# Performance work log

Measured on AMD Instinct MI355X. Metric: run time of the kernel, lower is better.

The kernel has to match this reference:

```python
import jax, jax.numpy as jnp
import numpy as np

N_VISITS, N_PROC, N_MED = 64, 32, 16
V_DIAG, V_PROC, V_MED = 2000, 1500, 4000
EMB, EMB_FF = 256, 128


def _normalize(adj):
    # row-normalize(adj + I), matching GCN.normalize
    adj = adj + np.eye(adj.shape[0], dtype=np.float32)
    rs = adj.sum(1)
    rinv = np.where(rs > 0, 1.0 / rs, 0.0).astype(np.float32)
    return (adj * rinv[:, None]).astype(np.float32)


def setup_inputs() -> dict:
    key = jax.random.key(0)
    ks = jax.random.split(key, 24)
    rng = np.random.default_rng(0)
    ehr = (rng.random((V_MED, V_MED)) < 0.01).astype(np.float32)
    ddi = (rng.random((V_MED, V_MED)) < 0.01).astype(np.float32)
    s = 0.02
    return {
        'proc_codes': jax.random.randint(ks[0], (N_VISITS, N_PROC), 0, V_DIAG + V_PROC + 2),
        'med_codes': jax.random.randint(ks[1], (N_VISITS, N_MED), 0, V_MED),
        'emb_table': jax.random.normal(ks[2], (V_DIAG + V_PROC + 2, EMB_FF)) * s,
        'conv_w': jax.random.normal(ks[3], (3,)) * 0.3,
        'conv_b': jnp.zeros((1,)),
        'wq': jax.random.normal(ks[4], (EMB_FF, EMB)) * s,
        'wk': jax.random.normal(ks[5], (EMB_FF, EMB)) * s,
        'wv': jax.random.normal(ks[6], (EMB_FF, EMB)) * s,
        'wr': jax.random.normal(ks[7], (EMB, EMB)) * s,
        'alpha': jax.random.normal(ks[8], (EMB,)),
        'beta': jax.random.normal(ks[9], (EMB,)),
        'ehr_adj_norm': jnp.asarray(_normalize(ehr)),
        'ddi_adj_norm': jnp.asarray(_normalize(ddi)),
        'ddi_adj_raw': jnp.asarray(ddi),
        'ehr_w1': jax.random.normal(ks[10], (V_MED, EMB)) * s,
        'ehr_b1': jnp.zeros((EMB,)),
        'ehr_w2': jax.random.normal(ks[11], (EMB, EMB)) * s,
        'ehr_b2': jnp.zeros((EMB,)),
        'ddi_w1': jax.random.normal(ks[12], (V_MED, EMB)) * s,
        'ddi_b1': jnp.zeros((EMB,)),
        'ddi_w2': jax.random.normal(ks[13], (EMB, EMB)) * s,
        'ddi_b2': jnp.zeros((EMB,)),
        'inter': jax.random.normal(ks[14], (1,)) * 0.1,
        'out_w1': jax.random.normal(ks[15], (3 * EMB, 2 * EMB)) * s,
        'out_b1': jnp.zeros((2 * EMB,)),
        'out_w2': jax.random.normal(ks[16], (2 * EMB, V_MED)) * s,
        'out_b2': jnp.zeros((V_MED,)),
    }


def _fastformer(x, wq, wk, wv, wr, alpha, beta):
    # x: (1, n, EMB_FF); additive linear attention (all-ones mask => no-op)
    q = x @ wq  # (1, n, EMB)
    k = x @ wk
    v = x @ wv
    scale = EMB ** -0.5
    aw = jax.nn.softmax(q * alpha * scale, axis=-1)
    gq = jnp.sum(q * aw, axis=1)              # global query (1, EMB)
    p = gq[:, None, :] * k                    # (1, n, EMB)
    bw = jax.nn.softmax(p * beta * scale, axis=-1)
    gk = jnp.sum(p * bw, axis=1)              # global key (1, EMB)
    return (gk[:, None, :] * v) @ wr + q


def _gcn(adj, w1, b1, w2, b2):
    # input x = I, so first layer support is just w1
    h = jax.nn.relu(adj @ w1 + b1)
    return adj @ (h @ w2) + b2


def reference(proc_codes, med_codes, emb_table, conv_w, conv_b, wq, wk, wv, wr, alpha, beta,
              ehr_adj_norm, ddi_adj_norm, ddi_adj_raw,
              ehr_w1, ehr_b1, ehr_w2, ehr_b2, ddi_w1, ddi_b1, ddi_w2, ddi_b2,
              inter, out_w1, out_b1, out_w2, out_b2):
    n = proc_codes.shape[0]
    # per-admission mean embedding  (n, EMB_FF)
    i2 = emb_table[proc_codes].mean(axis=1)
    # Conv1d(1,1,k=3,same) over the feature dim, then ReLU
    xp = jnp.pad(i2, ((0, 0), (1, 1)))
    i2 = jax.nn.relu(conv_w[0] * xp[:, :-2] + conv_w[1] * xp[:, 1:-1] + conv_w[2] * xp[:, 2:] + conv_b)
    feat = _fastformer(i2[None], wq, wk, wv, wr, alpha, beta)[0]  # (n, EMB)
    query = feat[-1:]
    drug_memory = _gcn(ehr_adj_norm, ehr_w1, ehr_b1, ehr_w2, ehr_b2) \
        - _gcn(ddi_adj_norm, ddi_w1, ddi_b1, ddi_w2, ddi_b2) * inter[0]
    key_w1 = jax.nn.softmax(query @ drug_memory.T, axis=-1)   # (1, V_MED)
    fact1 = key_w1 @ drug_memory                              # (1, EMB)
    # history (len(input) > 1): multi-hot med history values
    history_keys = feat[:-1]
    hv = jnp.zeros((n - 1, V_MED), dtype=feat.dtype)
    hv = hv.at[jnp.arange(n - 1)[:, None], med_codes[:-1]].set(1.0)
    visit_w = jax.nn.softmax(query @ history_keys.T, axis=-1)
    fact2 = (visit_w @ hv) @ drug_memory
    h = jnp.concatenate([query, fact1, fact2], axis=-1)       # (1, 3*EMB)
    result = jax.nn.relu(h @ out_w1 + out_b1) @ out_w2 + out_b2
    sp = jax.nn.sigmoid(result)[0]
    batch_neg = 0.0005 * jnp.einsum('i,ij,j->', sp, ddi_adj_raw, sp)
    return result, batch_neg
```

## Files before the change

kernel.cpp:

```cpp
#include <hip/hip_runtime.h>
#include <hip/hip_bf16.h>

#define NV 64
#define NP 32
#define NM 16
#define VMED 4000
#define EMB 256
#define EMBFF 128
#define CAP 128


__device__ __forceinline__ float block_sum_256(float v, float* red) {
    int t = threadIdx.x;
    red[t] = v; __syncthreads();
    for (int s = 128; s > 0; s >>= 1) { if (t < s) red[t] += red[t + s]; __syncthreads(); }
    float r = red[0]; __syncthreads();
    return r;
}
__device__ __forceinline__ float block_max_256(float v, float* red) {
    int t = threadIdx.x;
    red[t] = v; __syncthreads();
    for (int s = 128; s > 0; s >>= 1) { if (t < s) red[t] = fmaxf(red[t], red[t + s]); __syncthreads(); }
    float r = red[0]; __syncthreads();
    return r;
}

__global__ void k_ff1(const int* __restrict__ proc, const float* __restrict__ emb,
                      const float* __restrict__ cw, const float* __restrict__ cb,
                      const float* __restrict__ wq, const float* __restrict__ wk,
                      const float* __restrict__ wv, const float* __restrict__ alpha,
                      float* __restrict__ q, float* __restrict__ k, float* __restrict__ v,
                      float* __restrict__ qaw) {
    __shared__ float sm[EMBFF + 2];
    __shared__ float x[EMBFF];
    __shared__ float red[256];
    int vi = blockIdx.x, t = threadIdx.x;
    if (t < EMBFF) {
        float s = 0.f;
        for (int c = 0; c < NP; c++) s += emb[proc[vi * NP + c] * EMBFF + t];
        sm[t + 1] = s * (1.0f / NP);
    }
    if (t == 0) { sm[0] = 0.f; sm[EMBFF + 1] = 0.f; }
    __syncthreads();
    if (t < EMBFF) {
        float o = cw[0] * sm[t] + cw[1] * sm[t + 1] + cw[2] * sm[t + 2] + cb[0];
        x[t] = o > 0.f ? o : 0.f;
    }
    __syncthreads();
    float aq = 0, ak = 0, av = 0;
    for (int e = 0; e < EMBFF; e++) {
        float xe = x[e];
        aq += xe * wq[e * EMB + t];
        ak += xe * wk[e * EMB + t];
        av += xe * wv[e * EMB + t];
    }
    q[vi * EMB + t] = aq; k[vi * EMB + t] = ak; v[vi * EMB + t] = av;
    const float scale = 0.0625f;
    float z = aq * alpha[t] * scale;
    float m = block_max_256(z, red);
    float e_ = __expf(z - m);
    float sum = block_sum_256(e_, red);
    qaw[vi * EMB + t] = aq * (e_ / sum);
}

__global__ void k_pbw(const float* __restrict__ qaw, const float* __restrict__ k,
                      const float* __restrict__ beta, float* __restrict__ pbw) {
    __shared__ float red[256];
    int vi = blockIdx.x, f = threadIdx.x;
    float g = 0;
    for (int r = 0; r < NV; r++) g += qaw[r * EMB + f];
    float p = g * k[vi * EMB + f];
    const float scale = 0.0625f;
    float z = p * beta[f] * scale;
    float m = block_max_256(z, red);
    float e_ = __expf(z - m);
    float sum = block_sum_256(e_, red);
    pbw[vi * EMB + f] = p * (e_ / sum);
}

__global__ void k_feat(const float* __restrict__ pbw, const float* __restrict__ v,
                       const float* __restrict__ q, const float* __restrict__ wr,
                       float* __restrict__ feat) {
    __shared__ float s[EMB];
    int vi = blockIdx.x, f = threadIdx.x;
    float g = 0;
    for (int r = 0; r < NV; r++) g += pbw[r * EMB + f];
    s[f] = g * v[vi * EMB + f];
    __syncthreads();
    float acc = 0;
    for (int e = 0; e < EMB; e++) acc += s[e] * wr[e * EMB + f];
    feat[vi * EMB + f] = acc + q[vi * EMB + f];
}

__global__ void k_visitw_wmed(const float* __restrict__ feat, const int* __restrict__ med,
                              float* __restrict__ w_med) {
    __shared__ float qs[EMB];
    __shared__ float vw[64];
    __shared__ float red[256];
    __shared__ float wm[VMED];
    int t = threadIdx.x;
    for (int e = t; e < EMB; e += 256) qs[e] = feat[63 * EMB + e];
    for (int i = t; i < VMED; i += 256) wm[i] = 0.f;
    __syncthreads();
    float sc = -1e30f;
    if (t < 63) {
        float a = 0;
        for (int e = 0; e < EMB; e++) a += qs[e] * feat[t * EMB + e];
        sc = a;
    }
    float m = block_max_256(sc, red);
    float e_ = (t < 63) ? __expf(sc - m) : 0.f;
    float sum = block_sum_256(e_, red);
    if (t < 63) vw[t] = e_ / sum;
    __syncthreads();
    for (int i = t; i < 63 * NM; i += 256) {
        int vv = i / NM, mm = i % NM;
        int code = med[vv * NM + mm];
        bool dup = false;
        for (int m2 = 0; m2 < mm; m2++)
            if (med[vv * NM + m2] == code) dup = true;
        if (!dup) atomicAdd(&wm[code], vw[vv]);
    }
    __syncthreads();
    for (int i = t; i < VMED; i += 256) w_med[i] = wm[i];
}

__global__ void k_scan(const float* __restrict__ eadj, const float* __restrict__ draw,
                       int* __restrict__ ccntE, int* __restrict__ cidxE, float* __restrict__ cvalE,
                       int* __restrict__ ccntD, int* __restrict__ cidxD, float* __restrict__ cvalD) {
    __shared__ int idx[CAP];
    __shared__ float val[CAP];
    __shared__ int cnt;
    int b = blockIdx.x, t = threadIdx.x;
    bool isD = b >= VMED;
    int i = isD ? b - VMED : b;
    const float* adj = isD ? draw : eadj;
    int*   ccnt = isD ? ccntD : ccntE;
    int*   cidx = isD ? cidxD : cidxE;
    float* cval = isD ? cvalD : cvalE;
    if (t == 0) cnt = 0;
    const float4* row4 = (const float4*)(adj + (size_t)i * VMED);
    float4 a0 = row4[t];
    float4 a1 = row4[t + 256];
    float4 a2 = row4[t + 512];
    float4 a3 = (t < VMED / 4 - 768) ? row4[t + 768] : make_float4(0.f, 0.f, 0.f, 0.f);
    asm volatile("" :: "v"(a0.x), "v"(a0.y), "v"(a0.z), "v"(a0.w),
                       "v"(a1.x), "v"(a1.y), "v"(a1.z), "v"(a1.w),
                       "v"(a2.x), "v"(a2.y), "v"(a2.z), "v"(a2.w),
                       "v"(a3.x), "v"(a3.y), "v"(a3.z), "v"(a3.w));
    __syncthreads();
    #define PROC(A, C0) \
        if (A.x != 0.f) { int p = atomicAdd(&cnt, 1); if (p < CAP) { idx[p] = (C0);     val[p] = A.x; } } \
        if (A.y != 0.f) { int p = atomicAdd(&cnt, 1); if (p < CAP) { idx[p] = (C0) + 1; val[p] = A.y; } } \
        if (A.z != 0.f) { int p = atomicAdd(&cnt, 1); if (p < CAP) { idx[p] = (C0) + 2; val[p] = A.z; } } \
        if (A.w != 0.f) { int p = atomicAdd(&cnt, 1); if (p < CAP) { idx[p] = (C0) + 3; val[p] = A.w; } }
    PROC(a0, t * 4)
    PROC(a1, (t + 256) * 4)
    PROC(a2, (t + 512) * 4)
    PROC(a3, (t + 768) * 4)
    #undef PROC
    __syncthreads();
    int n;
    float rinv = 0.f;
    if (isD) {
        int n_raw = cnt < CAP - 1 ? cnt : CAP - 1;
        n = n_raw + 1;
        rinv = 1.0f / (float)n;
        if (t == n_raw) { idx[t] = i; }
    } else {
        n = cnt < CAP ? cnt : CAP;
    }
    __syncthreads();
    int n8 = (n + 7) & ~7;
    if (t == 0) ccnt[i] = n;
    if (t < n)       { cidx[i * CAP + t] = idx[t]; cval[i * CAP + t] = isD ? rinv : val[t]; }
    else if (t < n8) { cidx[i * CAP + t] = 0;      cval[i * CAP + t] = 0.f; }
}

__global__ void k_gat(const int* __restrict__ ccntE, const int* __restrict__ cidxE,
                      const float* __restrict__ cvalE,
                      const int* __restrict__ ccntD, const int* __restrict__ cidxD,
                      const float* __restrict__ cvalD,
                      const float* __restrict__ ew1, const float* __restrict__ eb1,
                      const float* __restrict__ dw1, const float* __restrict__ db1,
                      float* __restrict__ hE, float* __restrict__ hD) {
    int b = blockIdx.x, t = threadIdx.x;
    bool isD = (b & 4) != 0;
    int rank = (b >> 3) * 4 + (b & 3);
    const int*   ccnt = isD ? ccntD : ccntE;
    const int*   cidx = isD ? cidxD : cidxE;
    const float* cval = isD ? cvalD : cvalE;
    const float* w1   = isD ? dw1 : ew1;
    const float* b1   = isD ? db1 : eb1;
    float* h = isD ? hD : hE;
    int r0 = rank * 4;
    for (int r = 0; r < 4; r++) {
        int base = (r0 + r) * CAP;
        int n8 = (ccnt[r0 + r] + 7) & ~7;
        float acc = b1[t];
        for (int e = 0; e < n8; e += 8) {
            int i0 = cidx[base + e];     float v0 = cval[base + e];
            int i1 = cidx[base + e + 1]; float v1 = cval[base + e + 1];
            int i2 = cidx[base + e + 2]; float v2 = cval[base + e + 2];
            int i3 = cidx[base + e + 3]; float v3 = cval[base + e + 3];
            int i4 = cidx[base + e + 4]; float v4 = cval[base + e + 4];
            int i5 = cidx[base + e + 5]; float v5 = cval[base + e + 5];
            int i6 = cidx[base + e + 6]; float v6 = cval[base + e + 6];
            int i7 = cidx[base + e + 7]; float v7 = cval[base + e + 7];
            acc += v0 * w1[(size_t)i0 * EMB + t] + v1 * w1[(size_t)i1 * EMB + t]
                 + v2 * w1[(size_t)i2 * EMB + t] + v3 * w1[(size_t)i3 * EMB + t]
                 + v4 * w1[(size_t)i4 * EMB + t] + v5 * w1[(size_t)i5 * EMB + t]
                 + v6 * w1[(size_t)i6 * EMB + t] + v7 * w1[(size_t)i7 * EMB + t];
        }
        h[(size_t)(r0 + r) * EMB + t] = acc > 0.f ? acc : 0.f;
    }
}

__global__ void k_gemm2(const float* __restrict__ ew2, const float* __restrict__ dw2,
                        float* __restrict__ hE, float* __restrict__ hD) {
    __shared__ __align__(16) float x[EMB][12];
    int b = blockIdx.x, t = threadIdx.x;
    bool isD = (b & 4) != 0;
    int rank = (b >> 3) * 4 + (b & 3);
    const float* w2 = isD ? dw2 : ew2;
    float* h = isD ? hD : hE;
    int r0 = rank * 8;
    #pragma unroll
    for (int rr = 0; rr < 8; rr++)
        x[t][rr] = h[(size_t)(r0 + rr) * EMB + t];
    __syncthreads();
    float a0 = 0, a1 = 0, a2 = 0, a3 = 0, a4 = 0, a5 = 0, a6 = 0, a7 = 0;
    #pragma unroll 4
    for (int e = 0; e < EMB; e++) {
        float we = w2[e * EMB + t];
        float4 xa = *(const float4*)&x[e][0];
        float4 xb = *(const float4*)&x[e][4];
        a0 += xa.x * we; a1 += xa.y * we; a2 += xa.z * we; a3 += xa.w * we;
        a4 += xb.x * we; a5 += xb.y * we; a6 += xb.z * we; a7 += xb.w * we;
    }
    h[(size_t)(r0 + 0) * EMB + t] = a0;
    h[(size_t)(r0 + 1) * EMB + t] = a1;
    h[(size_t)(r0 + 2) * EMB + t] = a2;
    h[(size_t)(r0 + 3) * EMB + t] = a3;
    h[(size_t)(r0 + 4) * EMB + t] = a4;
    h[(size_t)(r0 + 5) * EMB + t] = a5;
    h[(size_t)(r0 + 6) * EMB + t] = a6;
    h[(size_t)(r0 + 7) * EMB + t] = a7;
}

__global__ void k_accE(const int* __restrict__ ccntE, const int* __restrict__ cidxE,
                       const float* __restrict__ cvalE, const float* __restrict__ xe,
                       const float* __restrict__ b2e, float* __restrict__ dm) {
    __shared__ int idxE[CAP];
    __shared__ float valE[CAP];
    int i = blockIdx.x, t = threadIdx.x;
    int nE = ccntE[i];
    int nE8 = (nE + 7) & ~7;
    if (t < nE) { idxE[t] = cidxE[i * CAP + t]; valE[t] = cvalE[i * CAP + t]; }
    else if (t < nE8) { idxE[t] = 0; valE[t] = 0.f; }
    __syncthreads();
    float aE = b2e[t];
    for (int e = 0; e < nE8; e += 8) {
        float g0 = xe[(size_t)idxE[e]     * EMB + t];
        float g1 = xe[(size_t)idxE[e + 1] * EMB + t];
        float g2 = xe[(size_t)idxE[e + 2] * EMB + t];
        float g3 = xe[(size_t)idxE[e + 3] * EMB + t];
        float g4 = xe[(size_t)idxE[e + 4] * EMB + t];
        float g5 = xe[(size_t)idxE[e + 5] * EMB + t];
        float g6 = xe[(size_t)idxE[e + 6] * EMB + t];
        float g7 = xe[(size_t)idxE[e + 7] * EMB + t];
        aE += valE[e] * g0 + valE[e + 1] * g1 + valE[e + 2] * g2 + valE[e + 3] * g3
            + valE[e + 4] * g4 + valE[e + 5] * g5 + valE[e + 6] * g6 + valE[e + 7] * g7;
    }
    dm[(size_t)i * EMB + t] = aE;
}

__global__ void k_accD(const int* __restrict__ ccntD, const int* __restrict__ cidxD,
                       const float* __restrict__ cvalD, const float* __restrict__ xd,
                       const float* __restrict__ b2d, const float* __restrict__ inter,
                       const float* __restrict__ feat, float* __restrict__ dm,
                       float* __restrict__ sdm) {
    __shared__ int idxD[CAP];
    __shared__ float valD[CAP];
    __shared__ float red[256];
    int i = blockIdx.x, t = threadIdx.x;
    int nD = ccntD[i];
    int nD8 = (nD + 7) & ~7;
    if (t < nD) { idxD[t] = cidxD[i * CAP + t]; valD[t] = cvalD[i * CAP + t]; }
    else if (t < nD8) { idxD[t] = 0; valD[t] = 0.f; }
    __syncthreads();
    float aD = b2d[t];
    for (int e = 0; e < nD8; e += 8) {
        float g0 = xd[(size_t)idxD[e]     * EMB + t];
        float g1 = xd[(size_t)idxD[e + 1] * EMB + t];
        float g2 = xd[(size_t)idxD[e + 2] * EMB + t];
        float g3 = xd[(size_t)idxD[e + 3] * EMB + t];
        float g4 = xd[(size_t)idxD[e + 4] * EMB + t];
        float g5 = xd[(size_t)idxD[e + 5] * EMB + t];
        float g6 = xd[(size_t)idxD[e + 6] * EMB + t];
        float g7 = xd[(size_t)idxD[e + 7] * EMB + t];
        aD += valD[e] * g0 + valD[e + 1] * g1 + valD[e + 2] * g2 + valD[e + 3] * g3
            + valD[e + 4] * g4 + valD[e + 5] * g5 + valD[e + 6] * g6 + valD[e + 7] * g7;
    }
    float dmv = dm[(size_t)i * EMB + t] - inter[0] * aD;
    dm[(size_t)i * EMB + t] = dmv;
    float s = block_sum_256(dmv * feat[63 * EMB + t], red);
    if (t == 0) sdm[i] = s;
}

__global__ void k_softmax4000(const float* __restrict__ s, float* __restrict__ out) {
    __shared__ float red[256];
    int t = threadIdx.x;
    float m = -1e30f;
    for (int i = t; i < VMED; i += 256) m = fmaxf(m, s[i]);
    m = block_max_256(m, red);
    float sum = 0;
    for (int i = t; i < VMED; i += 256) { float e = __expf(s[i] - m); out[i] = e; sum += e; }
    sum = block_sum_256(sum, red);
    float inv = 1.f / sum;
    for (int i = t; i < VMED; i += 256) out[i] *= inv;
}

__global__ void k_facts_part(const float* __restrict__ dm, const float* __restrict__ kw,
                             const float* __restrict__ wm, float* __restrict__ part1,
                             float* __restrict__ part2) {
    int f = threadIdx.x, b = blockIdx.x;
    int r0 = b * 100;
    float a1 = 0, a2 = 0;
    for (int r = r0; r < r0 + 100; r++) {
        float d = dm[(size_t)r * EMB + f];
        a1 += kw[r] * d;
        a2 += wm[r] * d;
    }
    part1[b * EMB + f] = a1;
    part2[b * EMB + f] = a2;
}

__global__ void k_hidden_part(const float* __restrict__ feat, const float* __restrict__ part1,
                              const float* __restrict__ part2, const float* __restrict__ w1,
                              float* __restrict__ hpart) {
    __shared__ float xs[16];
    int b = blockIdx.x, t = threadIdx.x;
    int e0 = b * 16;
    if (t < 16) {
        int e = e0 + t;
        float xv;
        if (e < 256) xv = feat[63 * EMB + e];
        else if (e < 512) { float s = 0; for (int p = 0; p < 40; p++) s += part1[p * EMB + (e - 256)]; xv = s; }
        else              { float s = 0; for (int p = 0; p < 40; p++) s += part2[p * EMB + (e - 512)]; xv = s; }
        xs[t] = xv;
    }
    __syncthreads();
    float a1 = 0, a2 = 0;
    #pragma unroll
    for (int i = 0; i < 16; i++) {
        int e = e0 + i;
        a1 += xs[i] * w1[e * 512 + t];
        a2 += xs[i] * w1[e * 512 + t + 256];
    }
    hpart[b * 512 + t] = a1;
    hpart[b * 512 + t + 256] = a2;
}

__global__ void k_result(const float* __restrict__ hpart, const float* __restrict__ b1,
                         const float* __restrict__ w2, const float* __restrict__ b2,
                         float* __restrict__ out, float* __restrict__ sp) {
    __shared__ float hx[512];
    __shared__ float red[8][32];
    int t = threadIdx.x;
    for (int jj = t; jj < 512; jj += 256) {
        float s = b1[jj];
        for (int p = 0; p < 48; p++) s += hpart[p * 512 + jj];
        hx[jj] = s > 0.f ? s : 0.f;
    }
    __syncthreads();
    int lane = t & 31, seg = t >> 5;
    int j = blockIdx.x * 32 + lane;
    float acc = 0;
    int e0 = seg * 64;
    #pragma unroll 8
    for (int e = e0; e < e0 + 64; e++) acc += hx[e] * w2[(size_t)e * VMED + j];
    red[seg][lane] = acc;
    __syncthreads();
    if (seg == 0) {
        float s = b2[j];
        for (int p = 0; p < 8; p++) s += red[p][lane];
        out[j] = s;
        sp[j] = 1.f / (1.f + __expf(-s));
    }
}

__global__ void k_bneg(const int* __restrict__ ccntD, const int* __restrict__ cidxD,
                       const float* __restrict__ sp, float* __restrict__ bpart) {
    int wv = threadIdx.x >> 6, lane = threadIdx.x & 63;
    int i = blockIdx.x * 4 + wv;
    int n = ccntD[i] - 1;
    float s = 0.f;
    for (int e = lane; e < n; e += 64) s += sp[cidxD[i * CAP + e]];
    for (int off = 32; off > 0; off >>= 1) s += __shfl_down(s, off, 64);
    if (lane == 0) bpart[i] = sp[i] * s;
}

__global__ void FastRx_wo_Diag_19473381720179_kernel(const float* __restrict__ bpart,
                                                     float* __restrict__ out) {
    __shared__ float red[256];
    int t = threadIdx.x;
    float s = 0;
    for (int i = t; i < VMED; i += 256) s += bpart[i];
    s = block_sum_256(s, red);
    if (t == 0) out[VMED] = 0.0005f * s;
}

extern "C" __attribute__((visibility("default")))
void kernel_launch(void* const* d_in, const int* in_sizes, int n_in,
                   void* d_out, int out_size, void* d_ws, size_t ws_size,
                   hipStream_t stream) {
    const int*   proc_codes = (const int*)d_in[0];
    const int*   med_codes  = (const int*)d_in[1];
    const float* emb_table  = (const float*)d_in[2];
    const float* conv_w     = (const float*)d_in[3];
    const float* conv_b     = (const float*)d_in[4];
    const float* wq         = (const float*)d_in[5];
    const float* wk         = (const float*)d_in[6];
    const float* wv         = (const float*)d_in[7];
    const float* wr         = (const float*)d_in[8];
    const float* alpha      = (const float*)d_in[9];
    const float* beta       = (const float*)d_in[10];
    const float* ehr_adj    = (const float*)d_in[11];
    const float* ddi_adj    = (const float*)d_in[12];
    const float* ddi_raw    = (const float*)d_in[13];
    const float* ehr_w1     = (const float*)d_in[14];
    const float* ehr_b1     = (const float*)d_in[15];
    const float* ehr_w2     = (const float*)d_in[16];
    const float* ehr_b2     = (const float*)d_in[17];
    const float* ddi_w1     = (const float*)d_in[18];
    const float* ddi_b1     = (const float*)d_in[19];
    const float* ddi_w2     = (const float*)d_in[20];
    const float* ddi_b2     = (const float*)d_in[21];
    const float* inter      = (const float*)d_in[22];
    const float* out_w1     = (const float*)d_in[23];
    const float* out_b1     = (const float*)d_in[24];
    const float* out_w2     = (const float*)d_in[25];
    const float* out_b2     = (const float*)d_in[26];
    float* out = (float*)d_out;

    float* w = (float*)d_ws;
    float* q      = w;
    float* k      = w + 16384;
    float* v      = w + 32768;
    float* tmpA   = w + 49152;
    float* tmpB   = w + 65536;
    float* feat   = w + 81920;
    float* wmed   = w + 98304;
    float* sdm    = w + 102400;
    float* sp     = w + 106496;
    float* bufA   = w + 110592;
    float* bufC   = bufA + 1024000;
    float* bufB   = bufC + 1024000;
    int*   ccntE  = (int*)(bufB + 1024000);
    int*   cidxE  = ccntE + 4096;
    float* cvalE  = (float*)(cidxE + 512000);
    int*   ccntD  = (int*)(cvalE + 512000);
    int*   cidxD  = ccntD + 4096;
    float* cvalD  = (float*)(cidxD + 512000);
    float* part1  = bufA;
    float* part2  = bufA + 10240;
    float* hpart  = bufA + 20480;
    float* bpart  = bufA + 45056;

    k_ff1<<<NV, EMB, 0, stream>>>(proc_codes, emb_table, conv_w, conv_b,
                                  wq, wk, wv, alpha, q, k, v, tmpA);
    k_pbw<<<NV, EMB, 0, stream>>>(tmpA, k, beta, tmpB);
    k_feat<<<NV, EMB, 0, stream>>>(tmpB, v, q, wr, feat);
    k_visitw_wmed<<<1, 256, 0, stream>>>(feat, med_codes, wmed);

    k_scan<<<2 * VMED, 256, 0, stream>>>(ehr_adj, ddi_raw,
                                         ccntE, cidxE, cvalE, ccntD, cidxD, cvalD);
    k_gat<<<2000, 256, 0, stream>>>(ccntE, cidxE, cvalE, ccntD, cidxD, cvalD,
                                    ehr_w1, ehr_b1, ddi_w1, ddi_b1,
                                    bufA, bufC);
    k_gemm2<<<1000, 256, 0, stream>>>(ehr_w2, ddi_w2, bufA, bufC);
    k_accE<<<VMED, 256, 0, stream>>>(ccntE, cidxE, cvalE, bufA, ehr_b2, bufB);
    k_accD<<<VMED, 256, 0, stream>>>(ccntD, cidxD, cvalD, bufC, ddi_b2, inter,
                                     feat, bufB, sdm);

    k_softmax4000<<<1, 256, 0, stream>>>(sdm, sdm);
    k_facts_part<<<40, 256, 0, stream>>>(bufB, sdm, wmed, part1, part2);
    k_hidden_part<<<48, 256, 0, stream>>>(feat, part1, part2, out_w1, hpart);
    k_result<<<125, 256, 0, stream>>>(hpart, out_b1, out_w2, out_b2, out, sp);
    k_bneg<<<VMED / 4, 256, 0, stream>>>(ccntD, cidxD, sp, bpart);
    FastRx_wo_Diag_19473381720179_kernel<<<1, 256, 0, stream>>>(bpart, out);
}
```

Before: 396.4 us.

## Merge front and tail kernel chains into cooperative kernels with grid sync

The four fastformer/visit-weight kernels become one cooperative kernel that uses grid.sync between stages. The six tail kernels (softmax, facts, hidden, result, bneg, final reduce) become one cooperative kernel of 125 blocks. The separate E and D accumulation kernels are fused into one, which also drops a dm write and reread. The goal is to cut launch overhead and inter-kernel gaps for many tiny kernels, at the price of grid-wide barrier cost, fewer blocks on some stages, and larger shared memory in the front kernel.

```diff
diff --git a/kernel.cpp b/kernel.cpp
--- a/kernel.cpp
+++ b/kernel.cpp
@@ -1,5 +1,8 @@
 #include <hip/hip_runtime.h>
 #include <hip/hip_bf16.h>
+#include <hip/hip_cooperative_groups.h>
+
+namespace cg = cooperative_groups;
 
 #define NV 64
 #define NP 32
@@ -25,16 +28,25 @@
     return r;
 }
 
-__global__ void k_ff1(const int* __restrict__ proc, const float* __restrict__ emb,
-                      const float* __restrict__ cw, const float* __restrict__ cb,
-                      const float* __restrict__ wq, const float* __restrict__ wk,
-                      const float* __restrict__ wv, const float* __restrict__ alpha,
-                      float* __restrict__ q, float* __restrict__ k, float* __restrict__ v,
-                      float* __restrict__ qaw) {
+__global__ void k_front(const int* __restrict__ proc, const float* __restrict__ emb,
+                        const float* __restrict__ cw, const float* __restrict__ cb,
+                        const float* __restrict__ wq, const float* __restrict__ wk,
+                        const float* __restrict__ wv, const float* __restrict__ alpha,
+                        const float* __restrict__ beta, const float* __restrict__ wr,
+                        const int* __restrict__ med,
+                        float* __restrict__ q, float* __restrict__ k, float* __restrict__ v,
+                        float* __restrict__ qaw, float* __restrict__ pbw,
+                        float* __restrict__ feat, float* __restrict__ w_med) {
     __shared__ float sm[EMBFF + 2];
     __shared__ float x[EMBFF];
     __shared__ float red[256];
+    __shared__ float sfeat[EMB];
+    __shared__ float qs[EMB];
+    __shared__ float vw[64];
+    __shared__ float wm[VMED];
+    cg::grid_group grid = cg::this_grid();
     int vi = blockIdx.x, t = threadIdx.x;
+
     if (t < EMBFF) {
         float s = 0.f;
         for (int c = 0; c < NP; c++) s += emb[proc[vi * NP + c] * EMBFF + t];
@@ -47,82 +59,74 @@
         x[t] = o > 0.f ? o : 0.f;
     }
     __syncthreads();
-    float aq = 0, ak = 0, av = 0;
-    for (int e = 0; e < EMBFF; e++) {
-        float xe = x[e];
-        aq += xe * wq[e * EMB + t];
-        ak += xe * wk[e * EMB + t];
-        av += xe * wv[e * EMB + t];
-    }
-    q[vi * EMB + t] = aq; k[vi * EMB + t] = ak; v[vi * EMB + t] = av;
-    const float scale = 0.0625f;
-    float z = aq * alpha[t] * scale;
-    float m = block_max_256(z, red);
-    float e_ = __expf(z - m);
-    float sum = block_sum_256(e_, red);
-    qaw[vi * EMB + t] = aq * (e_ / sum);
-}
-
-__global__ void k_pbw(const float* __restrict__ qaw, const float* __restrict__ k,
-                      const float* __restrict__ beta, float* __restrict__ pbw) {
-    __shared__ float red[256];
-    int vi = blockIdx.x, f = threadIdx.x;
-    float g = 0;
-    for (int r = 0; r < NV; r++) g += qaw[r * EMB + f];
-    float p = g * k[vi * EMB + f];
-    const float scale = 0.0625f;
-    float z = p * beta[f] * scale;
-    float m = block_max_256(z, red);
-    float e_ = __expf(z - m);
-    float sum = block_sum_256(e_, red);
-    pbw[vi * EMB + f] = p * (e_ / sum);
-}
-
-__global__ void k_feat(const float* __restrict__ pbw, const float* __restrict__ v,
-                       const float* __restrict__ q, const float* __restrict__ wr,
-                       float* __restrict__ feat) {
-    __shared__ float s[EMB];
-    int vi = blockIdx.x, f = threadIdx.x;
-    float g = 0;
-    for (int r = 0; r < NV; r++) g += pbw[r * EMB + f];
-    s[f] = g * v[vi * EMB + f];
-    __syncthreads();
-    float acc = 0;
-    for (int e = 0; e < EMB; e++) acc += s[e] * wr[e * EMB + f];
-    feat[vi * EMB + f] = acc + q[vi * EMB + f];
-}
-
-__global__ void k_visitw_wmed(const float* __restrict__ feat, const int* __restrict__ med,
-                              float* __restrict__ w_med) {
-    __shared__ float qs[EMB];
-    __shared__ float vw[64];
-    __shared__ float red[256];
-    __shared__ float wm[VMED];
-    int t = threadIdx.x;
-    for (int e = t; e < EMB; e += 256) qs[e] = feat[63 * EMB + e];
-    for (int i = t; i < VMED; i += 256) wm[i] = 0.f;
-    __syncthreads();
-    float sc = -1e30f;
-    if (t < 63) {
-        float a = 0;
-        for (int e = 0; e < EMB; e++) a += qs[e] * feat[t * EMB + e];
-        sc = a;
-    }
-    float m = block_max_256(sc, red);
-    float e_ = (t < 63) ? __expf(sc - m) : 0.f;
-    float sum = block_sum_256(e_, red);
-    if (t < 63) vw[t] = e_ / sum;
-    __syncthreads();
-    for (int i = t; i < 63 * NM; i += 256) {
-        int vv = i / NM, mm = i % NM;
-        int code = med[vv * NM + mm];
-        bool dup = false;
-        for (int m2 = 0; m2 < mm; m2++)
-            if (med[vv * NM + m2] == code) dup = true;
-        if (!dup) atomicAdd(&wm[code], vw[vv]);
-    }
-    __syncthreads();
-    for (int i = t; i < VMED; i += 256) w_med[i] = wm[i];
+    {
+        float aq = 0, ak = 0, av = 0;
+        for (int e = 0; e < EMBFF; e++) {
+            float xe = x[e];
+            aq += xe * wq[e * EMB + t];
+            ak += xe * wk[e * EMB + t];
+            av += xe * wv[e * EMB + t];
+        }
+        q[vi * EMB + t] = aq; k[vi * EMB + t] = ak; v[vi * EMB + t] = av;
+        const float scale = 0.0625f;
+        float z = aq * alpha[t] * scale;
+        float m = block_max_256(z, red);
+        float e_ = __expf(z - m);
+        float sum = block_sum_256(e_, red);
+        qaw[vi * EMB + t] = aq * (e_ / sum);
+    }
+    grid.sync();
+
+    {
+        float g = 0;
+        for (int r = 0; r < NV; r++) g += qaw[r * EMB + t];
+        float p = g * k[vi * EMB + t];
+        const float scale = 0.0625f;
+        float z = p * beta[t] * scale;
+        float m = block_max_256(z, red);
+        float e_ = __expf(z - m);
+        float sum = block_sum_256(e_, red);
+        pbw[vi * EMB + t] = p * (e_ / sum);
+    }
+    grid.sync();
+
+    {
+        float g = 0;
+        for (int r = 0; r < NV; r++) g += pbw[r * EMB + t];
+        sfeat[t] = g * v[vi * EMB + t];
+        __syncthreads();
+        float acc = 0;
+        for (int e = 0; e < EMB; e++) acc += sfeat[e] * wr[e * EMB + t];
+        feat[vi * EMB + t] = acc + q[vi * EMB + t];
+    }
+    grid.sync();
+
+    if (blockIdx.x == 0) {
+        for (int e = t; e < EMB; e += 256) qs[e] = feat[63 * EMB + e];
+        for (int i = t; i < VMED; i += 256) wm[i] = 0.f;
+        __syncthreads();
+        float sc = -1e30f;
+        if (t < 63) {
+            float a = 0;
+            for (int e = 0; e < EMB; e++) a += qs[e] * feat[t * EMB + e];
+            sc = a;
+        }
+        float m = block_max_256(sc, red);
+        float e_ = (t < 63) ? __expf(sc - m) : 0.f;
+        float sum = block_sum_256(e_, red);
+        if (t < 63) vw[t] = e_ / sum;
+        __syncthreads();
+        for (int i = t; i < 63 * NM; i += 256) {
+            int vv = i / NM, mm = i % NM;
+            int code = med[vv * NM + mm];
+            bool dup = false;
+            for (int m2 = 0; m2 < mm; m2++)
+                if (med[vv * NM + m2] == code) dup = true;
+            if (!dup) atomicAdd(&wm[code], vw[vv]);
+        }
+        __syncthreads();
+        for (int i = t; i < VMED; i += 256) w_med[i] = wm[i];
+    }
 }
 
 __global__ void k_scan(const float* __restrict__ eadj, const float* __restrict__ draw,
@@ -248,16 +252,28 @@
     h[(size_t)(r0 + 7) * EMB + t] = a7;
 }
 
-__global__ void k_accE(const int* __restrict__ ccntE, const int* __restrict__ cidxE,
-                       const float* __restrict__ cvalE, const float* __restrict__ xe,
-                       const float* __restrict__ b2e, float* __restrict__ dm) {
+__global__ void k_acc(const int* __restrict__ ccntE, const int* __restrict__ cidxE,
+                      const float* __restrict__ cvalE, const float* __restrict__ xe,
+                      const float* __restrict__ b2e,
+                      const int* __restrict__ ccntD, const int* __restrict__ cidxD,
+                      const float* __restrict__ cvalD, const float* __restrict__ xd,
+                      const float* __restrict__ b2d, const float* __restrict__ inter,
+                      const float* __restrict__ feat, float* __restrict__ dm,
+                      float* __restrict__ sdm) {
     __shared__ int idxE[CAP];
     __shared__ float valE[CAP];
+    __shared__ int idxD[CAP];
+    __shared__ float valD[CAP];
+    __shared__ float red[256];
     int i = blockIdx.x, t = threadIdx.x;
     int nE = ccntE[i];
     int nE8 = (nE + 7) & ~7;
     if (t < nE) { idxE[t] = cidxE[i * CAP + t]; valE[t] = cvalE[i * CAP + t]; }
     else if (t < nE8) { idxE[t] = 0; valE[t] = 0.f; }
+    int nD = ccntD[i];
+    int nD8 = (nD + 7) & ~7;
+    if (t < nD) { idxD[t] = cidxD[i * CAP + t]; valD[t] = cvalD[i * CAP + t]; }
+    else if (t < nD8) { idxD[t] = 0; valD[t] = 0.f; }
     __syncthreads();
     float aE = b2e[t];
     for (int e = 0; e < nE8; e += 8) {
@@ -272,23 +288,6 @@
         aE += valE[e] * g0 + valE[e + 1] * g1 + valE[e + 2] * g2 + valE[e + 3] * g3
             + valE[e + 4] * g4 + valE[e + 5] * g5 + valE[e + 6] * g6 + valE[e + 7] * g7;
     }
-    dm[(size_t)i * EMB + t] = aE;
-}
-
-__global__ void k_accD(const int* __restrict__ ccntD, const int* __restrict__ cidxD,
-                       const float* __restrict__ cvalD, const float* __restrict__ xd,
-                       const float* __restrict__ b2d, const float* __restrict__ inter,
-                       const float* __restrict__ feat, float* __restrict__ dm,
-                       float* __restrict__ sdm) {
-    __shared__ int idxD[CAP];
-    __shared__ float valD[CAP];
-    __shared__ float red[256];
-    int i = blockIdx.x, t = threadIdx.x;
-    int nD = ccntD[i];
-    int nD8 = (nD + 7) & ~7;
-    if (t < nD) { idxD[t] = cidxD[i * CAP + t]; valD[t] = cvalD[i * CAP + t]; }
-    else if (t < nD8) { idxD[t] = 0; valD[t] = 0.f; }
-    __syncthreads();
     float aD = b2d[t];
     for (int e = 0; e < nD8; e += 8) {
         float g0 = xd[(size_t)idxD[e]     * EMB + t];
@@ -302,113 +301,119 @@
         aD += valD[e] * g0 + valD[e + 1] * g1 + valD[e + 2] * g2 + valD[e + 3] * g3
             + valD[e + 4] * g4 + valD[e + 5] * g5 + valD[e + 6] * g6 + valD[e + 7] * g7;
     }
-    float dmv = dm[(size_t)i * EMB + t] - inter[0] * aD;
+    float dmv = aE - inter[0] * aD;
     dm[(size_t)i * EMB + t] = dmv;
     float s = block_sum_256(dmv * feat[63 * EMB + t], red);
     if (t == 0) sdm[i] = s;
 }
 
-__global__ void k_softmax4000(const float* __restrict__ s, float* __restrict__ out) {
+__global__ void FastRx_wo_Diag_19473381720179_kernel(
+        const float* __restrict__ dm, float* __restrict__ sdm,
+        const float* __restrict__ wm, const float* __restrict__ feat,
+        const float* __restrict__ ow1, const float* __restrict__ ob1,
+        const float* __restrict__ ow2, const float* __restrict__ ob2,
+        const int* __restrict__ ccntD, const int* __restrict__ cidxD,
+        float* __restrict__ part1, float* __restrict__ part2,
+        float* __restrict__ hpart, float* __restrict__ bpart,
+        float* __restrict__ out, float* __restrict__ sp) {
     __shared__ float red[256];
-    int t = threadIdx.x;
-    float m = -1e30f;
-    for (int i = t; i < VMED; i += 256) m = fmaxf(m, s[i]);
-    m = block_max_256(m, red);
-    float sum = 0;
-    for (int i = t; i < VMED; i += 256) { float e = __expf(s[i] - m); out[i] = e; sum += e; }
-    sum = block_sum_256(sum, red);
-    float inv = 1.f / sum;
-    for (int i = t; i < VMED; i += 256) out[i] *= inv;
-}
-
-__global__ void k_facts_part(const float* __restrict__ dm, const float* __restrict__ kw,
-                             const float* __restrict__ wm, float* __restrict__ part1,
-                             float* __restrict__ part2) {
-    int f = threadIdx.x, b = blockIdx.x;
-    int r0 = b * 100;
-    float a1 = 0, a2 = 0;
-    for (int r = r0; r < r0 + 100; r++) {
-        float d = dm[(size_t)r * EMB + f];
-        a1 += kw[r] * d;
-        a2 += wm[r] * d;
-    }
-    part1[b * EMB + f] = a1;
-    part2[b * EMB + f] = a2;
-}
-
-__global__ void k_hidden_part(const float* __restrict__ feat, const float* __restrict__ part1,
-                              const float* __restrict__ part2, const float* __restrict__ w1,
-                              float* __restrict__ hpart) {
     __shared__ float xs[16];
-    int b = blockIdx.x, t = threadIdx.x;
-    int e0 = b * 16;
-    if (t < 16) {
-        int e = e0 + t;
-        float xv;
-        if (e < 256) xv = feat[63 * EMB + e];
-        else if (e < 512) { float s = 0; for (int p = 0; p < 40; p++) s += part1[p * EMB + (e - 256)]; xv = s; }
-        else              { float s = 0; for (int p = 0; p < 40; p++) s += part2[p * EMB + (e - 512)]; xv = s; }
-        xs[t] = xv;
-    }
-    __syncthreads();
-    float a1 = 0, a2 = 0;
-    #pragma unroll
-    for (int i = 0; i < 16; i++) {
-        int e = e0 + i;
-        a1 += xs[i] * w1[e * 512 + t];
-        a2 += xs[i] * w1[e * 512 + t + 256];
-    }
-    hpart[b * 512 + t] = a1;
-    hpart[b * 512 + t + 256] = a2;
-}
-
-__global__ void k_result(const float* __restrict__ hpart, const float* __restrict__ b1,
-                         const float* __restrict__ w2, const float* __restrict__ b2,
-                         float* __restrict__ out, float* __restrict__ sp) {
     __shared__ float hx[512];
-    __shared__ float red[8][32];
-    int t = threadIdx.x;
-    for (int jj = t; jj < 512; jj += 256) {
-        float s = b1[jj];
-        for (int p = 0; p < 48; p++) s += hpart[p * 512 + jj];
-        hx[jj] = s > 0.f ? s : 0.f;
-    }
-    __syncthreads();
-    int lane = t & 31, seg = t >> 5;
-    int j = blockIdx.x * 32 + lane;
-    float acc = 0;
-    int e0 = seg * 64;
-    #pragma unroll 8
-    for (int e = e0; e < e0 + 64; e++) acc += hx[e] * w2[(size_t)e * VMED + j];
-    red[seg][lane] = acc;
-    __syncthreads();
-    if (seg == 0) {
-        float s = b2[j];
-        for (int p = 0; p < 8; p++) s += red[p][lane];
-        out[j] = s;
-        sp[j] = 1.f / (1.f + __expf(-s));
-    }
-}
-
-__global__ void k_bneg(const int* __restrict__ ccntD, const int* __restrict__ cidxD,
-                       const float* __restrict__ sp, float* __restrict__ bpart) {
-    int wv = threadIdx.x >> 6, lane = threadIdx.x & 63;
-    int i = blockIdx.x * 4 + wv;
-    int n = ccntD[i] - 1;
-    float s = 0.f;
-    for (int e = lane; e < n; e += 64) s += sp[cidxD[i * CAP + e]];
-    for (int off = 32; off > 0; off >>= 1) s += __shfl_down(s, off, 64);
-    if (lane == 0) bpart[i] = sp[i] * s;
-}
-
-__global__ void FastRx_wo_Diag_19473381720179_kernel(const float* __restrict__ bpart,
-                                                     float* __restrict__ out) {
-    __shared__ float red[256];
-    int t = threadIdx.x;
-    float s = 0;
-    for (int i = t; i < VMED; i += 256) s += bpart[i];
-    s = block_sum_256(s, red);
-    if (t == 0) out[VMED] = 0.0005f * s;
+    __shared__ float red8[8][32];
+    cg::grid_group grid = cg::this_grid();
+    int t = threadIdx.x, b = blockIdx.x;
+
+    if (b == 0) {
+        float m = -1e30f;
+        for (int i = t; i < VMED; i += 256) m = fmaxf(m, sdm[i]);
+        m = block_max_256(m, red);
+        float sum = 0;
+        for (int i = t; i < VMED; i += 256) { float e = __expf(sdm[i] - m); sdm[i] = e; sum += e; }
+        sum = block_sum_256(sum, red);
+        float inv = 1.f / sum;
+        for (int i = t; i < VMED; i += 256) sdm[i] *= inv;
+    }
+    grid.sync();
+
+    if (b < 40) {
+        int r0 = b * 100;
+        float a1 = 0, a2 = 0;
+        for (int r = r0; r < r0 + 100; r++) {
+            float d = dm[(size_t)r * EMB + t];
+            a1 += sdm[r] * d;
+            a2 += wm[r] * d;
+        }
+        part1[b * EMB + t] = a1;
+        part2[b * EMB + t] = a2;
+    }
+    grid.sync();
+
+    if (b < 48) {
+        int e0 = b * 16;
+        if (t < 16) {
+            int e = e0 + t;
+            float xv;
+            if (e < 256) xv = feat[63 * EMB + e];
+            else if (e < 512) { float s = 0; for (int p = 0; p < 40; p++) s += part1[p * EMB + (e - 256)]; xv = s; }
+            else              { float s = 0; for (int p = 0; p < 40; p++) s += part2[p * EMB + (e - 512)]; xv = s; }
+            xs[t] = xv;
+        }
+        __syncthreads();
+        float a1 = 0, a2 = 0;
+        #pragma unroll
+        for (int i = 0; i < 16; i++) {
+            int e = e0 + i;
+            a1 += xs[i] * ow1[e * 512 + t];
+            a2 += xs[i] * ow1[e * 512 + t + 256];
+        }
+        hpart[b * 512 + t] = a1;
+        hpart[b * 512 + t + 256] = a2;
+    }
+    grid.sync();
+
+    {
+        for (int jj = t; jj < 512; jj += 256) {
+            float s = ob1[jj];
+            for (int p = 0; p < 48; p++) s += hpart[p * 512 + jj];
+            hx[jj] = s > 0.f ? s : 0.f;
+        }
+        __syncthreads();
+        int lane = t & 31, seg = t >> 5;
+        int j = b * 32 + lane;
+        float acc = 0;
+        int e0 = seg * 64;
+        #pragma unroll 8
+        for (int e = e0; e < e0 + 64; e++) acc += hx[e] * ow2[(size_t)e * VMED + j];
+        red8[seg][lane] = acc;
+        __syncthreads();
+        if (seg == 0) {
+            float s = ob2[j];
+            for (int p = 0; p < 8; p++) s += red8[p][lane];
+            out[j] = s;
+            sp[j] = 1.f / (1.f + __expf(-s));
+        }
+    }
+    grid.sync();
+
+    {
+        int wv = t >> 6, lane = t & 63;
+        int wgl = b * 4 + wv;
+        for (int i = wgl; i < VMED; i += 500) {
+            int n = ccntD[i] - 1;
+            float s = 0.f;
+            for (int e = lane; e < n; e += 64) s += sp[cidxD[i * CAP + e]];
+            for (int off = 32; off > 0; off >>= 1) s += __shfl_down(s, off, 64);
+            if (lane == 0) bpart[i] = sp[i] * s;
+        }
+    }
+    grid.sync();
+
+    if (b == 0) {
+        float s = 0;
+        for (int i = t; i < VMED; i += 256) s += bpart[i];
+        s = block_sum_256(s, red);
+        if (t == 0) out[VMED] = 0.0005f * s;
+    }
 }
 
 extern "C" __attribute__((visibility("default")))
@@ -468,26 +473,31 @@
     float* hpart  = bufA + 20480;
     float* bpart  = bufA + 45056;
 
-    k_ff1<<<NV, EMB, 0, stream>>>(proc_codes, emb_table, conv_w, conv_b,
-                                  wq, wk, wv, alpha, q, k, v, tmpA);
-    k_pbw<<<NV, EMB, 0, stream>>>(tmpA, k, beta, tmpB);
-    k_feat<<<NV, EMB, 0, stream>>>(tmpB, v, q, wr, feat);
-    k_visitw_wmed<<<1, 256, 0, stream>>>(feat, med_codes, wmed);
-
+    {
+        void* args[] = {(void*)&proc_codes, (void*)&emb_table, (void*)&conv_w, (void*)&conv_b,
+                        (void*)&wq, (void*)&wk, (void*)&wv, (void*)&alpha, (void*)&beta,
+                        (void*)&wr, (void*)&med_codes,
+                        (void*)&q, (void*)&k, (void*)&v, (void*)&tmpA, (void*)&tmpB,
+                        (void*)&feat, (void*)&wmed};
+        hipLaunchCooperativeKernel((const void*)k_front, dim3(NV), dim3(EMB), args, 0, stream);
+    }
     k_scan<<<2 * VMED, 256, 0, stream>>>(ehr_adj, ddi_raw,
                                          ccntE, cidxE, cvalE, ccntD, cidxD, cvalD);
     k_gat<<<2000, 256, 0, stream>>>(ccntE, cidxE, cvalE, ccntD, cidxD, cvalD,
                                     ehr_w1, ehr_b1, ddi_w1, ddi_b1,
                                     bufA, bufC);
     k_gemm2<<<1000, 256, 0, stream>>>(ehr_w2, ddi_w2, bufA, bufC);
-    k_accE<<<VMED, 256, 0, stream>>>(ccntE, cidxE, cvalE, bufA, ehr_b2, bufB);
-    k_accD<<<VMED, 256, 0, stream>>>(ccntD, cidxD, cvalD, bufC, ddi_b2, inter,
-                                     feat, bufB, sdm);
-
-    k_softmax4000<<<1, 256, 0, stream>>>(sdm, sdm);
-    k_facts_part<<<40, 256, 0, stream>>>(bufB, sdm, wmed, part1, part2);
-    k_hidden_part<<<48, 256, 0, stream>>>(feat, part1, part2, out_w1, hpart);
-    k_result<<<125, 256, 0, stream>>>(hpart, out_b1, out_w2, out_b2, out, sp);
-    k_bneg<<<VMED / 4, 256, 0, stream>>>(ccntD, cidxD, sp, bpart);
-    FastRx_wo_Diag_19473381720179_kernel<<<1, 256, 0, stream>>>(bpart, out);
-}
+    k_acc<<<VMED, 256, 0, stream>>>(ccntE, cidxE, cvalE, bufA, ehr_b2,
+                                    ccntD, cidxD, cvalD, bufC, ddi_b2,
+                                    inter, feat, bufB, sdm);
+    {
+        const float* dm_c = bufB;
+        void* args[] = {(void*)&dm_c, (void*)&sdm, (void*)&wmed, (void*)&feat,
+                        (void*)&out_w1, (void*)&out_b1, (void*)&out_w2, (void*)&out_b2,
+                        (void*)&ccntD, (void*)&cidxD,
+                        (void*)&part1, (void*)&part2, (void*)&hpart, (void*)&bpart,
+                        (void*)&out, (void*)&sp};
+        hipLaunchCooperativeKernel((const void*)FastRx_wo_Diag_19473381720179_kernel,
+                                   dim3(125), dim3(256), args, 0, stream);
+    }
+}
```

Result: slower. 564.3 us (+42.4%).

## Avoid materializing drug_memory by reassociating GCN second layer with query and weights

Applied to the files above, without the earlier changes.

Instead of computing the full 4000x256 second GCN layer (gemm2 plus sparse aggregation) and then reducing it against the query and attention weights, the code projects the query through W2 first. It then computes per-row scalar scores via sparse dot products, scatters the softmax and history weights back through the adjacency transpose with atomics, and applies W2 only once to the weighted sums. This removes the dense 4000x256x256 GEMMs and the wide gathers, and adds several small kernels plus atomic scatter. Float atomics make the accumulation order nondeterministic.

```diff
diff --git a/kernel.cpp b/kernel.cpp
--- a/kernel.cpp
+++ b/kernel.cpp
@@ -123,6 +123,28 @@
     }
     __syncthreads();
     for (int i = t; i < VMED; i += 256) w_med[i] = wm[i];
+}
+
+__global__ void k_qproj(const float* __restrict__ ew2, const float* __restrict__ dw2,
+                        const float* __restrict__ b2e, const float* __restrict__ b2d,
+                        const float* __restrict__ feat,
+                        float* __restrict__ qE, float* __restrict__ qD,
+                        float* __restrict__ cc) {
+    __shared__ float red[256];
+    int b = blockIdx.x, t = threadIdx.x;
+    const float* q = feat + 63 * EMB;
+    float val;
+    if (b < 256)      val = ew2[b * EMB + t] * q[t];
+    else if (b < 512) val = dw2[(b - 256) * EMB + t] * q[t];
+    else if (b == 512) val = b2e[t] * q[t];
+    else               val = b2d[t] * q[t];
+    float s = block_sum_256(val, red);
+    if (t == 0) {
+        if (b < 256) qE[b] = s;
+        else if (b < 512) qD[b - 256] = s;
+        else if (b == 512) cc[0] = s;
+        else cc[1] = s;
+    }
 }
 
 __global__ void k_scan(const float* __restrict__ eadj, const float* __restrict__ draw,
@@ -216,96 +238,55 @@
     }
 }
 
-__global__ void k_gemm2(const float* __restrict__ ew2, const float* __restrict__ dw2,
-                        float* __restrict__ hE, float* __restrict__ hD) {
-    __shared__ __align__(16) float x[EMB][12];
+__global__ void k_u(const float* __restrict__ hE, const float* __restrict__ hD,
+                    const float* __restrict__ qE, const float* __restrict__ qD,
+                    const float* __restrict__ wm,
+                    float* __restrict__ uE, float* __restrict__ uD,
+                    float* __restrict__ vbuf, float* __restrict__ swm) {
+    __shared__ float red[256];
     int b = blockIdx.x, t = threadIdx.x;
-    bool isD = (b & 4) != 0;
-    int rank = (b >> 3) * 4 + (b & 3);
-    const float* w2 = isD ? dw2 : ew2;
-    float* h = isD ? hD : hE;
-    int r0 = rank * 8;
-    #pragma unroll
-    for (int rr = 0; rr < 8; rr++)
-        x[t][rr] = h[(size_t)(r0 + rr) * EMB + t];
-    __syncthreads();
-    float a0 = 0, a1 = 0, a2 = 0, a3 = 0, a4 = 0, a5 = 0, a6 = 0, a7 = 0;
-    #pragma unroll 4
-    for (int e = 0; e < EMB; e++) {
-        float we = w2[e * EMB + t];
-        float4 xa = *(const float4*)&x[e][0];
-        float4 xb = *(const float4*)&x[e][4];
-        a0 += xa.x * we; a1 += xa.y * we; a2 += xa.z * we; a3 += xa.w * we;
-        a4 += xb.x * we; a5 += xb.y * we; a6 += xb.z * we; a7 += xb.w * we;
-    }
-    h[(size_t)(r0 + 0) * EMB + t] = a0;
-    h[(size_t)(r0 + 1) * EMB + t] = a1;
-    h[(size_t)(r0 + 2) * EMB + t] = a2;
-    h[(size_t)(r0 + 3) * EMB + t] = a3;
-    h[(size_t)(r0 + 4) * EMB + t] = a4;
-    h[(size_t)(r0 + 5) * EMB + t] = a5;
-    h[(size_t)(r0 + 6) * EMB + t] = a6;
-    h[(size_t)(r0 + 7) * EMB + t] = a7;
-}
-
-__global__ void k_accE(const int* __restrict__ ccntE, const int* __restrict__ cidxE,
-                       const float* __restrict__ cvalE, const float* __restrict__ xe,
-                       const float* __restrict__ b2e, float* __restrict__ dm) {
-    __shared__ int idxE[CAP];
-    __shared__ float valE[CAP];
-    int i = blockIdx.x, t = threadIdx.x;
+    if (b < 2000) {
+        int w = t >> 6, lane = t & 63;
+        int j = b * 4 + w;
+        const float* row; const float* qv; float* uo;
+        if (j < VMED) { row = hE + (size_t)j * EMB; qv = qE; uo = uE + j; }
+        else { row = hD + (size_t)(j - VMED) * EMB; qv = qD; uo = uD + (j - VMED); }
+        float4 hv = *(const float4*)(row + lane * 4);
+        float4 qq = *(const float4*)(qv + lane * 4);
+        float s = hv.x * qq.x + hv.y * qq.y + hv.z * qq.z + hv.w * qq.w;
+        for (int off = 32; off > 0; off >>= 1) s += __shfl_down(s, off, 64);
+        if (lane == 0) *uo = s;
+    } else if (b < 2063) {
+        int idx = (b - 2000) * 256 + t;
+        if (idx < 16000) vbuf[idx] = 0.f;
+    } else {
+        float s = 0;
+        for (int i = t; i < VMED; i += 256) s += wm[i];
+        s = block_sum_256(s, red);
+        if (t == 0) swm[0] = s;
+    }
+}
+
+__global__ void k_sdm(const int* __restrict__ ccntE, const int* __restrict__ cidxE,
+                      const float* __restrict__ cvalE,
+                      const int* __restrict__ ccntD, const int* __restrict__ cidxD,
+                      const float* __restrict__ cvalD,
+                      const float* __restrict__ uE, const float* __restrict__ uD,
+                      const float* __restrict__ cc, const float* __restrict__ inter,
+                      float* __restrict__ sdm) {
+    int t = threadIdx.x;
+    int i = blockIdx.x * 4 + (t >> 6), lane = t & 63;
     int nE = ccntE[i];
-    int nE8 = (nE + 7) & ~7;
-    if (t < nE) { idxE[t] = cidxE[i * CAP + t]; valE[t] = cvalE[i * CAP + t]; }
-    else if (t < nE8) { idxE[t] = 0; valE[t] = 0.f; }
-    __syncthreads();
-    float aE = b2e[t];
-    for (int e = 0; e < nE8; e += 8) {
-        float g0 = xe[(size_t)idxE[e]     * EMB + t];
-        float g1 = xe[(size_t)idxE[e + 1] * EMB + t];
-        float g2 = xe[(size_t)idxE[e + 2] * EMB + t];
-        float g3 = xe[(size_t)idxE[e + 3] * EMB + t];
-        float g4 = xe[(size_t)idxE[e + 4] * EMB + t];
-        float g5 = xe[(size_t)idxE[e + 5] * EMB + t];
-        float g6 = xe[(size_t)idxE[e + 6] * EMB + t];
-        float g7 = xe[(size_t)idxE[e + 7] * EMB + t];
-        aE += valE[e] * g0 + valE[e + 1] * g1 + valE[e + 2] * g2 + valE[e + 3] * g3
-            + valE[e + 4] * g4 + valE[e + 5] * g5 + valE[e + 6] * g6 + valE[e + 7] * g7;
-    }
-    dm[(size_t)i * EMB + t] = aE;
-}
-
-__global__ void k_accD(const int* __restrict__ ccntD, const int* __restrict__ cidxD,
-                       const float* __restrict__ cvalD, const float* __restrict__ xd,
-                       const float* __restrict__ b2d, const float* __restrict__ inter,
-                       const float* __restrict__ feat, float* __restrict__ dm,
-                       float* __restrict__ sdm) {
-    __shared__ int idxD[CAP];
-    __shared__ float valD[CAP];
-    __shared__ float red[256];
-    int i = blockIdx.x, t = threadIdx.x;
+    float sE = 0.f;
+    for (int e = lane; e < nE; e += 64) sE += cvalE[i * CAP + e] * uE[cidxE[i * CAP + e]];
     int nD = ccntD[i];
-    int nD8 = (nD + 7) & ~7;
-    if (t < nD) { idxD[t] = cidxD[i * CAP + t]; valD[t] = cvalD[i * CAP + t]; }
-    else if (t < nD8) { idxD[t] = 0; valD[t] = 0.f; }
-    __syncthreads();
-    float aD = b2d[t];
-    for (int e = 0; e < nD8; e += 8) {
-        float g0 = xd[(size_t)idxD[e]     * EMB + t];
-        float g1 = xd[(size_t)idxD[e + 1] * EMB + t];
-        float g2 = xd[(size_t)idxD[e + 2] * EMB + t];
-        float g3 = xd[(size_t)idxD[e + 3] * EMB + t];
-        float g4 = xd[(size_t)idxD[e + 4] * EMB + t];
-        float g5 = xd[(size_t)idxD[e + 5] * EMB + t];
-        float g6 = xd[(size_t)idxD[e + 6] * EMB + t];
-        float g7 = xd[(size_t)idxD[e + 7] * EMB + t];
-        aD += valD[e] * g0 + valD[e + 1] * g1 + valD[e + 2] * g2 + valD[e + 3] * g3
-            + valD[e + 4] * g4 + valD[e + 5] * g5 + valD[e + 6] * g6 + valD[e + 7] * g7;
-    }
-    float dmv = dm[(size_t)i * EMB + t] - inter[0] * aD;
-    dm[(size_t)i * EMB + t] = dmv;
-    float s = block_sum_256(dmv * feat[63 * EMB + t], red);
-    if (t == 0) sdm[i] = s;
+    float sD = 0.f;
+    for (int e = lane; e < nD; e += 64) sD += cvalD[i * CAP + e] * uD[cidxD[i * CAP + e]];
+    for (int off = 32; off > 0; off >>= 1) {
+        sE += __shfl_down(sE, off, 64);
+        sD += __shfl_down(sD, off, 64);
+    }
+    if (lane == 0) sdm[i] = (sE + cc[0]) - inter[0] * (sD + cc[1]);
 }
 
 __global__ void k_softmax4000(const float* __restrict__ s, float* __restrict__ out) {
@@ -321,23 +302,77 @@
     for (int i = t; i < VMED; i += 256) out[i] *= inv;
 }
 
-__global__ void k_facts_part(const float* __restrict__ dm, const float* __restrict__ kw,
-                             const float* __restrict__ wm, float* __restrict__ part1,
-                             float* __restrict__ part2) {
+__global__ void k_scatter(const int* __restrict__ ccntE, const int* __restrict__ cidxE,
+                          const float* __restrict__ cvalE,
+                          const int* __restrict__ ccntD, const int* __restrict__ cidxD,
+                          const float* __restrict__ cvalD,
+                          const float* __restrict__ kw, const float* __restrict__ wm,
+                          float* __restrict__ vE, float* __restrict__ v2E,
+                          float* __restrict__ vD, float* __restrict__ v2D) {
+    int t = threadIdx.x;
+    int i = blockIdx.x * 4 + (t >> 6), lane = t & 63;
+    float kwi = kw[i], wmi = wm[i];
+    int nE = ccntE[i];
+    for (int e = lane; e < nE; e += 64) {
+        int j = cidxE[i * CAP + e];
+        float v = cvalE[i * CAP + e];
+        atomicAdd(&vE[j], kwi * v);
+        atomicAdd(&v2E[j], wmi * v);
+    }
+    int nD = ccntD[i];
+    for (int e = lane; e < nD; e += 64) {
+        int j = cidxD[i * CAP + e];
+        float v = cvalD[i * CAP + e];
+        atomicAdd(&vD[j], kwi * v);
+        atomicAdd(&v2D[j], wmi * v);
+    }
+}
+
+__global__ void k_wsum(const float* __restrict__ hE, const float* __restrict__ hD,
+                       const float* __restrict__ vE, const float* __restrict__ v2E,
+                       const float* __restrict__ vD, const float* __restrict__ v2D,
+                       float* __restrict__ pe1, float* __restrict__ pe2,
+                       float* __restrict__ pd1, float* __restrict__ pd2) {
     int f = threadIdx.x, b = blockIdx.x;
-    int r0 = b * 100;
-    float a1 = 0, a2 = 0;
-    for (int r = r0; r < r0 + 100; r++) {
-        float d = dm[(size_t)r * EMB + f];
-        a1 += kw[r] * d;
-        a2 += wm[r] * d;
-    }
-    part1[b * EMB + f] = a1;
-    part2[b * EMB + f] = a2;
-}
-
-__global__ void k_hidden_part(const float* __restrict__ feat, const float* __restrict__ part1,
-                              const float* __restrict__ part2, const float* __restrict__ w1,
+    float a1 = 0, a2 = 0, a3 = 0, a4 = 0;
+    int j0 = b * 100;
+    for (int j = j0; j < j0 + 100; j++) {
+        float he = hE[(size_t)j * EMB + f];
+        float hd = hD[(size_t)j * EMB + f];
+        a1 += vE[j] * he; a2 += v2E[j] * he;
+        a3 += vD[j] * hd; a4 += v2D[j] * hd;
+    }
+    pe1[b * EMB + f] = a1; pe2[b * EMB + f] = a2;
+    pd1[b * EMB + f] = a3; pd2[b * EMB + f] = a4;
+}
+
+__global__ void k_facts_final(const float* __restrict__ pe1, const float* __restrict__ pe2,
+                              const float* __restrict__ pd1, const float* __restrict__ pd2,
+                              const float* __restrict__ ew2, const float* __restrict__ dw2,
+                              const float* __restrict__ b2e, const float* __restrict__ b2d,
+                              const float* __restrict__ inter, const float* __restrict__ swm,
+                              float* __restrict__ fact1, float* __restrict__ fact2) {
+    __shared__ float gA[EMB];
+    __shared__ float gB[EMB];
+    int b = blockIdx.x, t = threadIdx.x;
+    const float* pa = (b == 0) ? pe1 : pe2;
+    const float* pb = (b == 0) ? pd1 : pd2;
+    float s1 = 0, s2 = 0;
+    for (int p = 0; p < 40; p++) { s1 += pa[p * EMB + t]; s2 += pb[p * EMB + t]; }
+    gA[t] = s1; gB[t] = s2;
+    __syncthreads();
+    float accE = 0, accD = 0;
+    for (int e = 0; e < EMB; e++) {
+        accE += gA[e] * ew2[e * EMB + t];
+        accD += gB[e] * dw2[e * EMB + t];
+    }
+    float bs = (b == 0) ? 1.f : swm[0];
+    float r = accE + bs * b2e[t] - inter[0] * (accD + bs * b2d[t]);
+    if (b == 0) fact1[t] = r; else fact2[t] = r;
+}
+
+__global__ void k_hidden_part(const float* __restrict__ feat, const float* __restrict__ fact1,
+                              const float* __restrict__ fact2, const float* __restrict__ w1,
                               float* __restrict__ hpart) {
     __shared__ float xs[16];
     int b = blockIdx.x, t = threadIdx.x;
@@ -346,8 +381,8 @@
         int e = e0 + t;
         float xv;
         if (e < 256) xv = feat[63 * EMB + e];
-        else if (e < 512) { float s = 0; for (int p = 0; p < 40; p++) s += part1[p * EMB + (e - 256)]; xv = s; }
-        else              { float s = 0; for (int p = 0; p < 40; p++) s += part2[p * EMB + (e - 512)]; xv = s; }
+        else if (e < 512) xv = fact1[e - 256];
+        else              xv = fact2[e - 512];
         xs[t] = xv;
     }
     __syncthreads();
@@ -463,8 +498,23 @@
     int*   ccntD  = (int*)(cvalE + 512000);
     int*   cidxD  = ccntD + 4096;
     float* cvalD  = (float*)(cidxD + 512000);
-    float* part1  = bufA;
-    float* part2  = bufA + 10240;
+    float* qE   = bufB;
+    float* qD   = bufB + 256;
+    float* cc   = bufB + 512;
+    float* swm  = bufB + 514;
+    float* uE   = bufB + 1024;
+    float* uD   = bufB + 5120;
+    float* vbuf = bufB + 10240;
+    float* vE   = vbuf;
+    float* v2E  = vbuf + 4000;
+    float* vD   = vbuf + 8000;
+    float* v2D  = vbuf + 12000;
+    float* pe1  = bufB + 26624;
+    float* pe2  = bufB + 36864;
+    float* pd1  = bufB + 47104;
+    float* pd2  = bufB + 57344;
+    float* fact1  = bufA;
+    float* fact2  = bufA + 256;
     float* hpart  = bufA + 20480;
     float* bpart  = bufA + 45056;
 
@@ -473,20 +523,23 @@
     k_pbw<<<NV, EMB, 0, stream>>>(tmpA, k, beta, tmpB);
     k_feat<<<NV, EMB, 0, stream>>>(tmpB, v, q, wr, feat);
     k_visitw_wmed<<<1, 256, 0, stream>>>(feat, med_codes, wmed);
+    k_qproj<<<514, 256, 0, stream>>>(ehr_w2, ddi_w2, ehr_b2, ddi_b2, feat, qE, qD, cc);
 
     k_scan<<<2 * VMED, 256, 0, stream>>>(ehr_adj, ddi_raw,
                                          ccntE, cidxE, cvalE, ccntD, cidxD, cvalD);
     k_gat<<<2000, 256, 0, stream>>>(ccntE, cidxE, cvalE, ccntD, cidxD, cvalD,
                                     ehr_w1, ehr_b1, ddi_w1, ddi_b1,
                                     bufA, bufC);
-    k_gemm2<<<1000, 256, 0, stream>>>(ehr_w2, ddi_w2, bufA, bufC);
-    k_accE<<<VMED, 256, 0, stream>>>(ccntE, cidxE, cvalE, bufA, ehr_b2, bufB);
-    k_accD<<<VMED, 256, 0, stream>>>(ccntD, cidxD, cvalD, bufC, ddi_b2, inter,
-                                     feat, bufB, sdm);
-
+    k_u<<<2064, 256, 0, stream>>>(bufA, bufC, qE, qD, wmed, uE, uD, vbuf, swm);
+    k_sdm<<<1000, 256, 0, stream>>>(ccntE, cidxE, cvalE, ccntD, cidxD, cvalD,
+                                    uE, uD, cc, inter, sdm);
     k_softmax4000<<<1, 256, 0, stream>>>(sdm, sdm);
-    k_facts_part<<<40, 256, 0, stream>>>(bufB, sdm, wmed, part1, part2);
-    k_hidden_part<<<48, 256, 0, stream>>>(feat, part1, part2, out_w1, hpart);
+    k_scatter<<<1000, 256, 0, stream>>>(ccntE, cidxE, cvalE, ccntD, cidxD, cvalD,
+                                        sdm, wmed, vE, v2E, vD, v2D);
+    k_wsum<<<40, 256, 0, stream>>>(bufA, bufC, vE, v2E, vD, v2D, pe1, pe2, pd1, pd2);
+    k_facts_final<<<2, 256, 0, stream>>>(pe1, pe2, pd1, pd2, ehr_w2, ddi_w2,
+                                         ehr_b2, ddi_b2, inter, swm, fact1, fact2);
+    k_hidden_part<<<48, 256, 0, stream>>>(feat, fact1, fact2, out_w1, hpart);
     k_result<<<125, 256, 0, stream>>>(hpart, out_b1, out_w2, out_b2, out, sp);
     k_bneg<<<VMED / 4, 256, 0, stream>>>(ccntD, cidxD, sp, bpart);
     FastRx_wo_Diag_19473381720179_kernel<<<1, 256, 0, stream>>>(bpart, out);
```

New measurement: 402.4 us. No clear change (+1.5%).
